# Optimization experiments

Measured on AMD Instinct MI355X. Metric: run time of the kernel, lower is better.

Reference implementation:

```python
import jax, jax.numpy as jnp
import numpy as np


def setup_inputs() -> dict:
    key = jax.random.key(0)
    kx, kw = jax.random.split(key)
    x = jax.random.normal(kx, (2, 64, 16, 128, 128), dtype=jnp.float32)
    # Conv3d(in=2, out=1, kernel=7, padding=3, bias=False) weight, OIDHW layout
    w = jax.random.normal(kw, (1, 2, 7, 7, 7), dtype=jnp.float32) * (1.0 / np.sqrt(2 * 7 * 7 * 7))
    return {"x": x, "w": w}


def reference(x, w):
    # x: (B, C, T, H, W); w: (O=1, I=2, 7, 7, 7)
    max_out = jnp.max(x, axis=1, keepdims=True)   # (B,1,T,H,W)
    avg_out = jnp.mean(x, axis=1, keepdims=True)  # (B,1,T,H,W)
    concat = jnp.concatenate([max_out, avg_out], axis=1)  # (B,2,T,H,W)
    conv = jax.lax.conv_general_dilated(
        concat, w,
        window_strides=(1, 1, 1),
        padding=[(3, 3), (3, 3), (3, 3)],
        dimension_numbers=("NCDHW", "OIDHW", "NCDHW"),
    )  # (B,1,T,H,W)
    attn = jax.nn.sigmoid(conv)
    return attn * x
```

## Files before the change

kernel.cpp:

```cpp
#include <hip/hip_runtime.h>
#include <math.h>


#define NP (2 * 16 * 128 * 128)

__global__ __launch_bounds__(256) void pool_kernel(const float* __restrict__ x,
                                                   float* __restrict__ pmax,
                                                   float* __restrict__ pavg) {
    int j = blockIdx.x * 256 + threadIdx.x;
    int b = j >> 16;
    int rest = j & 65535;
    const float4* x4 = (const float4*)x;
    int base = (b << 22) | rest;

    float4 v = x4[base];
    float4 vmax = v;
    float4 vsum = v;
#pragma unroll 8
    for (int c = 1; c < 64; ++c) {
        float4 u = x4[base + (c << 16)];
        vmax.x = fmaxf(vmax.x, u.x);
        vmax.y = fmaxf(vmax.y, u.y);
        vmax.z = fmaxf(vmax.z, u.z);
        vmax.w = fmaxf(vmax.w, u.w);
        vsum.x += u.x; vsum.y += u.y; vsum.z += u.z; vsum.w += u.w;
    }
    const float s = 1.0f / 64.0f;
    float4 vavg; vavg.x = vsum.x * s; vavg.y = vsum.y * s; vavg.z = vsum.z * s; vavg.w = vsum.w * s;
    ((float4*)pmax)[j] = vmax;
    ((float4*)pavg)[j] = vavg;
}

__global__ __launch_bounds__(256) void conv_kernel(const float* __restrict__ pooled,
                                                   const float* __restrict__ wgt,
                                                   float* __restrict__ attn) {
    __shared__ float sm[2 * 38 * 39];

    int bid = blockIdx.x;
    int tw0 = (bid & 3) << 5;
    int th0 = ((bid >> 2) & 3) << 5;
    int t = (bid >> 4) & 15;
    int b = bid >> 8;

    int tid = threadIdx.x;
    int ty = tid >> 3;
    int txg = (tid & 7) << 2;

    float acc0 = 0.f, acc1 = 0.f, acc2 = 0.f, acc3 = 0.f;

    for (int dz = 0; dz < 7; ++dz) {
        int tsrc = t + dz - 3;
        if (tsrc < 0 || tsrc >= 16) continue;

        __syncthreads();
        for (int i = tid; i < 2 * 38 * 38; i += 256) {
            int ch = i / 1444;
            int rem = i - ch * 1444;
            int y = rem / 38;
            int xx = rem - y * 38;
            int gh = th0 + y - 3;
            int gw = tw0 + xx - 3;
            float val = 0.f;
            if ((unsigned)gh < 128u && (unsigned)gw < 128u)
                val = pooled[ch * NP + (((b << 4) + tsrc) << 14) + (gh << 7) + gw];
            sm[ch * (38 * 39) + y * 39 + xx] = val;
        }
        __syncthreads();

        const float* wdz = wgt + dz * 49;
#pragma unroll
        for (int ch = 0; ch < 2; ++ch) {
#pragma unroll
            for (int dy = 0; dy < 7; ++dy) {
                const float* rp = &sm[ch * (38 * 39) + (ty + dy) * 39 + txg];
                float row[10];
#pragma unroll
                for (int k = 0; k < 10; ++k) row[k] = rp[k];
                const float* wr = wdz + ch * 343 + dy * 7;
#pragma unroll
                for (int dx = 0; dx < 7; ++dx) {
                    float wv = wr[dx];
                    acc0 = fmaf(wv, row[dx + 0], acc0);
                    acc1 = fmaf(wv, row[dx + 1], acc1);
                    acc2 = fmaf(wv, row[dx + 2], acc2);
                    acc3 = fmaf(wv, row[dx + 3], acc3);
                }
            }
        }
    }

    float4 o;
    o.x = 1.f / (1.f + expf(-acc0));
    o.y = 1.f / (1.f + expf(-acc1));
    o.z = 1.f / (1.f + expf(-acc2));
    o.w = 1.f / (1.f + expf(-acc3));
    int oi = (((b << 4) + t) << 14) + ((th0 + ty) << 7) + (tw0 + txg);
    *(float4*)(attn + oi) = o;
}

__global__ __launch_bounds__(256) void mul_kernel(const float* __restrict__ x,
                                                  const float* __restrict__ attn,
                                                  float* __restrict__ out) {
    int j = blockIdx.x * 256 + threadIdx.x;
    const float4* x4 = (const float4*)x;
    const float4* a4 = (const float4*)attn;
    float4 xv = x4[j];
    float4 av = a4[((j >> 22) << 16) | (j & 65535)];
    float4 o;
    o.x = xv.x * av.x;
    o.y = xv.y * av.y;
    o.z = xv.z * av.z;
    o.w = xv.w * av.w;
    ((float4*)out)[j] = o;
}

extern "C" void kernel_launch(void* const* d_in, const int* in_sizes, int n_in,
                              void* d_out, int out_size, void* d_ws, size_t ws_size,
                              hipStream_t stream) {
    const float* x = (const float*)d_in[0];
    const float* w = (const float*)d_in[1];
    float* out = (float*)d_out;
    float* ws = (float*)d_ws;

    float* pmax = ws;
    float* pavg = ws + NP;
    float* attn = ws + 2 * NP;

    pool_kernel<<<NP / 4 / 256, 256, 0, stream>>>(x, pmax, pavg);
    conv_kernel<<<2 * 16 * 4 * 4, 256, 0, stream>>>(pmax, w, attn);
    mul_kernel<<<(1 << 23) / 256, 256, 0, stream>>>(x, attn, out);
}
```

Before: 280.8 us.

## Fuse sigmoid-attention multiply into the conv kernel with nontemporal stores

Drops the separate elementwise multiply kernel and the attention buffer. Each conv thread now computes its four sigmoid values and loops over all 64 channels, loading x and writing the product with nontemporal stores. This removes one launch and the attention write and read-back. The cost is that the full 256 MB of x traffic now runs through only 512 blocks, so low occupancy may limit memory bandwidth, and the streaming work is serialised behind each block's conv compute.

```diff
diff --git a/kernel.cpp b/kernel.cpp
--- a/kernel.cpp
+++ b/kernel.cpp
@@ -3,6 +3,8 @@
 
 
 #define NP (2 * 16 * 128 * 128)
+
+typedef float vfloat4 __attribute__((ext_vector_type(4)));
 
 __global__ __launch_bounds__(256) void pool_kernel(const float* __restrict__ x,
                                                    float* __restrict__ pmax,
@@ -31,9 +33,10 @@
     ((float4*)pavg)[j] = vavg;
 }
 
-__global__ __launch_bounds__(256) void conv_kernel(const float* __restrict__ pooled,
-                                                   const float* __restrict__ wgt,
-                                                   float* __restrict__ attn) {
+__global__ __launch_bounds__(256) void conv_mul_kernel(const float* __restrict__ pooled,
+                                                       const float* __restrict__ wgt,
+                                                       const float* __restrict__ x,
+                                                       float* __restrict__ out) {
     __shared__ float sm[2 * 38 * 39];
 
     int bid = blockIdx.x;
@@ -89,29 +92,21 @@
         }
     }
 
-    float4 o;
-    o.x = 1.f / (1.f + expf(-acc0));
-    o.y = 1.f / (1.f + expf(-acc1));
-    o.z = 1.f / (1.f + expf(-acc2));
-    o.w = 1.f / (1.f + expf(-acc3));
-    int oi = (((b << 4) + t) << 14) + ((th0 + ty) << 7) + (tw0 + txg);
-    *(float4*)(attn + oi) = o;
-}
+    float a0 = 1.f / (1.f + expf(-acc0));
+    float a1 = 1.f / (1.f + expf(-acc1));
+    float a2 = 1.f / (1.f + expf(-acc2));
+    float a3 = 1.f / (1.f + expf(-acc3));
 
-__global__ __launch_bounds__(256) void mul_kernel(const float* __restrict__ x,
-                                                  const float* __restrict__ attn,
-                                                  float* __restrict__ out) {
-    int j = blockIdx.x * 256 + threadIdx.x;
-    const float4* x4 = (const float4*)x;
-    const float4* a4 = (const float4*)attn;
-    float4 xv = x4[j];
-    float4 av = a4[((j >> 22) << 16) | (j & 65535)];
-    float4 o;
-    o.x = xv.x * av.x;
-    o.y = xv.y * av.y;
-    o.z = xv.z * av.z;
-    o.w = xv.w * av.w;
-    ((float4*)out)[j] = o;
+    int base4 = (b << 22) + (t << 12) + ((th0 + ty) << 5) + ((tw0 + txg) >> 2);
+    const vfloat4* x4 = (const vfloat4*)x;
+    vfloat4* o4 = (vfloat4*)out;
+    vfloat4 av = {a0, a1, a2, a3};
+#pragma unroll 4
+    for (int c = 0; c < 64; ++c) {
+        int idx = base4 + (c << 16);
+        vfloat4 xv = x4[idx];
+        __builtin_nontemporal_store(xv * av, &o4[idx]);
+    }
 }
 
 extern "C" void kernel_launch(void* const* d_in, const int* in_sizes, int n_in,
@@ -124,9 +119,7 @@
 
     float* pmax = ws;
     float* pavg = ws + NP;
-    float* attn = ws + 2 * NP;
 
     pool_kernel<<<NP / 4 / 256, 256, 0, stream>>>(x, pmax, pavg);
-    conv_kernel<<<2 * 16 * 4 * 4, 256, 0, stream>>>(pmax, w, attn);
-    mul_kernel<<<(1 << 23) / 256, 256, 0, stream>>>(x, attn, out);
+    conv_mul_kernel<<<2 * 16 * 4 * 4, 256, 0, stream>>>(pmax, w, x, out);
 }
```

Result: faster. 273.3 us (-2.7%).
